# Optimization experiments

Measured on AMD Instinct MI355X. Metric: run time of the kernel, lower is better.

Reference implementation:

```python
import jax, jax.numpy as jnp
import numpy as np
from jax.scipy.linalg import solve_triangular

NUM_EMBEDDINGS = 512
EMBEDDING_DIM = 64
SPARSITY = 5
COMMITMENT = 0.25
EPS = 1e-10


def setup_inputs() -> dict:
    key = jax.random.key(0)
    k1, k2 = jax.random.split(key)
    z_e = jax.random.normal(k1, (64, EMBEDDING_DIM, 32, 32), dtype=jnp.float32)
    dictionary = jax.random.normal(k2, (EMBEDDING_DIM, NUM_EMBEDDINGS), dtype=jnp.float32)
    return {"z_e": z_e, "dictionary": dictionary}


def batch_omp(X, D, K):
    """Batched OMP with incremental Cholesky. X: (M, Bs), D: (M, N) col-normalized.
    Returns coefficients (N, Bs)."""
    N = D.shape[1]
    Bs = X.shape[1]
    G = D.T @ D                      # (N, N) Gram
    h_bar = (D.T @ X).T              # (Bs, N) correlations
    h = h_bar
    x = jnp.zeros_like(h_bar)        # dense coeff matrix, nonzero only on support
    I_logic = jnp.zeros((Bs, N), dtype=bool)
    L = jnp.ones((Bs, 1, 1), dtype=X.dtype)
    I = None
    b = jnp.arange(Bs)
    for k in range(1, K + 1):        # unrolled: K is a small static constant
        # pick most correlated unselected atom per sample
        index = jnp.argmax(jnp.abs(jnp.where(I_logic, 0.0, h)), axis=1)  # (Bs,)
        I_logic = I_logic.at[b, index].set(True)
        if k > 1:
            # incremental Cholesky update: L_new = [[L, 0], [w^T, sqrt(1 - |w|^2)]]
            G_stack = G[I, index[:, None]]                               # (Bs, k-1)
            w = solve_triangular(L, G_stack[..., None], lower=True)      # (Bs, k-1, 1)
            w_corner = jnp.sqrt(1.0 - jnp.sum(w ** 2, axis=1, keepdims=True))  # (Bs,1,1)
            top = jnp.concatenate([L, jnp.zeros((Bs, k - 1, 1), X.dtype)], axis=2)
            bot = jnp.concatenate([jnp.swapaxes(w, 1, 2), w_corner], axis=2)
            L = jnp.concatenate([top, bot], axis=1)                      # (Bs, k, k)
            I = jnp.concatenate([I, index[:, None]], axis=1)             # (Bs, k)
        else:
            I = index[:, None]
        # solve (L L^T) x_I = h_bar_I  (cholesky_solve)
        h_stack = jnp.take_along_axis(h_bar, I, axis=1)[..., None]       # (Bs, k, 1)
        y = solve_triangular(L, h_stack, lower=True)
        x_stack = solve_triangular(L, y, lower=True, trans=1)[..., 0]    # (Bs, k)
        # scatter support coefficients (indices are distinct per sample)
        x = jnp.zeros_like(h_bar).at[b[:, None], I].set(x_stack)
        beta = x @ G                                                     # (Bs, N)
        h = h_bar - beta
    return x.T                                                           # (N, Bs)


def reference(z_e, dictionary):
    B, C, H, W = z_e.shape
    signals = jnp.transpose(z_e, (0, 2, 3, 1)).reshape(-1, C).T          # (C, B*H*W)
    # F.normalize(dictionary, p=2, dim=0, eps)
    d_norm = dictionary / jnp.maximum(
        jnp.linalg.norm(dictionary, axis=0, keepdims=True), EPS)
    # sparse coding is done under no_grad in the original
    coeffs = jax.lax.stop_gradient(
        batch_omp(jax.lax.stop_gradient(signals),
                  jax.lax.stop_gradient(d_norm), SPARSITY))              # (N, B*H*W)
    recon = (d_norm @ coeffs).T                                          # (B*H*W, C)
    z_dl = jnp.transpose(recon.reshape(B, H, W, C), (0, 3, 1, 2))
    dl_latent_loss = jnp.mean((z_dl - jax.lax.stop_gradient(z_e)) ** 2)
    e_latent_loss = jnp.mean((jax.lax.stop_gradient(z_dl) - z_e) ** 2)
    loss = dl_latent_loss + COMMITMENT * e_latent_loss
    # straight-through estimator
    z_dl_st = z_e + jax.lax.stop_gradient(z_dl - z_e)
    return z_dl_st, loss, coeffs
```

## Files before the change

### kernel.cpp

```cpp
#include <hip/hip_runtime.h>
#include <type_traits>

#define N_ATOMS 512
#define C_DIM   64
#define K_SP    5
#define TS      16
#define HSTR    20


__global__ __launch_bounds__(256) void prep_norm_k(const float* __restrict__ dict,
                                                   float* __restrict__ dn,
                                                   float* __restrict__ dnT,
                                                   double* __restrict__ lossAcc) {
#pragma clang fp contract(off)
  const int n = blockIdx.x * 256 + threadIdx.x;
  if (blockIdx.x == 0 && threadIdx.x == 0) *lossAcc = 0.0;
  if (n >= N_ATOMS) return;
  float s = 0.0f;
  for (int c = 0; c < C_DIM; ++c) {
    float v = dict[c * N_ATOMS + n];
    float sq = v * v;
    s = s + sq;
  }
  float m = fmaxf(sqrtf(s), 1e-10f);
  for (int c = 0; c < C_DIM; ++c) {
    float q = dict[c * N_ATOMS + n] / m;
    dn[c * N_ATOMS + n] = q;
    dnT[n * C_DIM + c] = q;
  }
}

__global__ __launch_bounds__(256) void prep_gram_k(const float* __restrict__ dn,
                                                   float* __restrict__ G) {
#pragma clang fp contract(off)
  __shared__ float As[64][64];
  __shared__ float Bs[64][64];
  const int bi = blockIdx.x & 7, bj = blockIdx.x >> 3;
  const int tid = threadIdx.x;
  for (int r = 0; r < 16; ++r) {
    int e = r * 256 + tid;
    int c = e >> 6, i = e & 63;
    As[c][i] = dn[c * N_ATOMS + bi * 64 + i];
    Bs[c][i] = dn[c * N_ATOMS + bj * 64 + i];
  }
  __syncthreads();
  const int ti = tid & 15, tj = tid >> 4;
  float acc[4][4] = {};
  for (int c = 0; c < 64; ++c) {
    float a[4], b[4];
#pragma unroll
    for (int u = 0; u < 4; ++u) { a[u] = As[c][ti * 4 + u]; b[u] = Bs[c][tj * 4 + u]; }
#pragma unroll
    for (int u = 0; u < 4; ++u)
#pragma unroll
      for (int v = 0; v < 4; ++v) acc[u][v] = fmaf(a[u], b[v], acc[u][v]);
  }
  for (int u = 0; u < 4; ++u)
    for (int v = 0; v < 4; ++v)
      G[(size_t)(bi * 64 + ti * 4 + u) * N_ATOMS + bj * 64 + tj * 4 + v] = acc[u][v];
}

__global__ __launch_bounds__(256) void omp_main_k(const float* __restrict__ z,
                                                  const float* __restrict__ dn,
                                                  const float* __restrict__ dnT,
                                                  const float* __restrict__ Gm,
                                                  float* __restrict__ out0,
                                                  float* __restrict__ coeffs,
                                                  double* __restrict__ lossAcc) {
#pragma clang fp contract(off)
  __shared__ float Xs[64][16];
  __shared__ __align__(16) float UB[N_ATOMS * HSTR];
  __shared__ int   IldsI[TS][K_SP];
  __shared__ float IldsX[TS][K_SP];

  const int tid   = threadIdx.x;
  const int sbase = blockIdx.x * TS;
  const int b     = sbase >> 10;
  const int hw0   = sbase & 1023;
  const float* zb = z + (size_t)b * 65536;

  {
    int c = tid >> 2, slc = (tid & 3) * 4;
    float4 v = *reinterpret_cast<const float4*>(zb + c * 1024 + hw0 + slc);
    *reinterpret_cast<float4*>(&Xs[c][slc]) = v;
  }

  const int ia4 = (tid & 63) * 4;
  const int js4 = (tid >> 6) * 4;
  float acc[8][4] = {};
#pragma unroll
  for (int cc = 0; cc < 4; ++cc) {
    __syncthreads();
    {
      const float* src = dn + cc * 8192;
#pragma unroll
      for (int r = 0; r < 8; ++r) {
        int off = (r * 256 + tid) * 4;
        *reinterpret_cast<float4*>(&UB[off]) = *reinterpret_cast<const float4*>(src + off);
      }
    }
    __syncthreads();
#pragma unroll
    for (int c = 0; c < 16; ++c) {
      const float4 xv = *reinterpret_cast<const float4*>(&Xs[cc * 16 + c][js4]);
      const float4 d0 = *reinterpret_cast<const float4*>(&UB[c * 512 + ia4]);
      const float4 d1 = *reinterpret_cast<const float4*>(&UB[c * 512 + 256 + ia4]);
      const float dv[8] = { d0.x, d0.y, d0.z, d0.w, d1.x, d1.y, d1.z, d1.w };
      const float xw[4] = { xv.x, xv.y, xv.z, xv.w };
#pragma unroll
      for (int r = 0; r < 8; ++r)
#pragma unroll
        for (int u = 0; u < 4; ++u)
          acc[r][u] = fmaf(dv[r], xw[u], acc[r][u]);
    }
  }
  __syncthreads();
#pragma unroll
  for (int r = 0; r < 8; ++r) {
    int n = (r < 4) ? (ia4 + r) : (256 + ia4 + (r - 4));
    *reinterpret_cast<float4*>(&UB[n * HSTR + js4]) =
        make_float4(acc[r][0], acc[r][1], acc[r][2], acc[r][3]);
  }
  __syncthreads();

  const int lane = tid & 63;
  const int wid  = tid >> 6;
  double lsum = 0.0;

  for (int q = 0; q < 4; ++q) {
    const int sl = wid * 4 + q;
    float hb[8];
#pragma unroll
    for (int jb = 0; jb < 8; ++jb) hb[jb] = UB[(lane + 64 * jb) * HSTR + sl];

    unsigned selmask = 0;
    int   I[K_SP];
    float xs[K_SP];
    float hstk[K_SP];
    float Lm[K_SP][K_SP];
    int   srtI[4];
    float GrowS[4][8];

    auto iter = [&](auto KC) {
      constexpr int k = decltype(KC)::value;
      float cur[8];
      if constexpr (k == 1) {
#pragma unroll
        for (int jb = 0; jb < 8; ++jb) cur[jb] = hb[jb];
      } else {
        float xsS[k - 1];
#pragma unroll
        for (int u = 0; u < k - 1; ++u) {
          float xv = 0.0f;
#pragma unroll
          for (int t = 0; t < k - 1; ++t) xv = (I[t] == srtI[u]) ? xs[t] : xv;
          xsS[u] = xv;
        }
#pragma unroll
        for (int jb = 0; jb < 8; ++jb) {
          float beta = 0.0f;
#pragma unroll
          for (int u = 0; u < k - 1; ++u) beta = fmaf(xsS[u], GrowS[u][jb], beta);
          cur[jb] = hb[jb] - beta;
        }
      }
      float bv = -1.0f; int bn = 1 << 30;
#pragma unroll
      for (int jb = 0; jb < 8; ++jb) {
        float v = ((selmask >> jb) & 1u) ? 0.0f : fabsf(cur[jb]);
        int n = lane + 64 * jb;
        bool better = (v > bv) || ((v == bv) && (n < bn));
        bv = better ? v : bv; bn = better ? n : bn;
      }
#pragma unroll
      for (int m = 1; m < 64; m <<= 1) {
        float ov = __shfl_xor(bv, m, 64);
        int   on = __shfl_xor(bn, m, 64);
        bool better = (ov > bv) || ((ov == bv) && (on < bn));
        bv = better ? ov : bv; bn = better ? on : bn;
      }
      const int nsel = bn;
      I[k - 1] = nsel;
      if ((nsel & 63) == lane) selmask |= (1u << (nsel >> 6));

      if constexpr (k > 1) {
        float Gs[k - 1], w[k - 1];
#pragma unroll
        for (int t = 0; t < k - 1; ++t) Gs[t] = Gm[(size_t)I[t] * N_ATOMS + nsel];
#pragma unroll
        for (int t = 0; t < k - 1; ++t) {
          float a = Gs[t];
#pragma unroll
          for (int u = 0; u < t; ++u) a = a - Lm[t][u] * w[u];
          w[t] = a / Lm[t][t];
        }
        float ss = 0.0f;
#pragma unroll
        for (int t = 0; t < k - 1; ++t) { float sq = w[t] * w[t]; ss = ss + sq; }
        float wc = sqrtf(1.0f - ss);
#pragma unroll
        for (int t = 0; t < k - 1; ++t) Lm[k - 1][t] = w[t];
        Lm[k - 1][k - 1] = wc;
      } else {
        Lm[0][0] = 1.0f;
      }
      hstk[k - 1] = UB[nsel * HSTR + sl];
      float y[k];
#pragma unroll
      for (int t = 0; t < k; ++t) {
        float a = hstk[t];
#pragma unroll
        for (int u = 0; u < t; ++u) a = a - Lm[t][u] * y[u];
        y[t] = a / Lm[t][t];
      }
#pragma unroll
      for (int t = k - 1; t >= 0; --t) {
        float a = y[t];
#pragma unroll
        for (int u = t + 1; u < k; ++u) a = a - Lm[u][t] * xs[u];
        xs[t] = a / Lm[t][t];
      }
      if constexpr (k <= 4) {
        float nr[8];
#pragma unroll
        for (int jb = 0; jb < 8; ++jb) nr[jb] = Gm[(size_t)nsel * N_ATOMS + lane + 64 * jb];
        int p = 0;
#pragma unroll
        for (int u = 0; u < k - 1; ++u) p += (srtI[u] < nsel) ? 1 : 0;
#pragma unroll
        for (int u = k - 1; u >= 1; --u) {
          bool tp = (u > p);
          srtI[u] = tp ? srtI[u - 1] : srtI[u];
#pragma unroll
          for (int jb = 0; jb < 8; ++jb) GrowS[u][jb] = tp ? GrowS[u - 1][jb] : GrowS[u][jb];
        }
#pragma unroll
        for (int u = 0; u < k; ++u) {
          bool at = (u == p);
          srtI[u] = at ? nsel : srtI[u];
#pragma unroll
          for (int jb = 0; jb < 8; ++jb) GrowS[u][jb] = at ? nr[jb] : GrowS[u][jb];
        }
      }
    };
    iter(std::integral_constant<int, 1>{});
    iter(std::integral_constant<int, 2>{});
    iter(std::integral_constant<int, 3>{});
    iter(std::integral_constant<int, 4>{});
    iter(std::integral_constant<int, 5>{});

    if (lane == 0) {
#pragma unroll
      for (int t = 0; t < K_SP; ++t) { IldsI[sl][t] = I[t]; IldsX[sl][t] = xs[t]; }
    }

    int sI[5]; float sX[5];
#pragma unroll
    for (int t = 0; t < 5; ++t) { sI[t] = I[t]; sX[t] = xs[t]; }
#pragma unroll
    for (int a = 0; a < 4; ++a)
#pragma unroll
      for (int t = 0; t < 4 - a; ++t) {
        bool sw = sI[t] > sI[t + 1];
        int   i0 = sw ? sI[t + 1] : sI[t];
        int   i1 = sw ? sI[t] : sI[t + 1];
        float x0 = sw ? sX[t + 1] : sX[t];
        float x1 = sw ? sX[t] : sX[t + 1];
        sI[t] = i0; sI[t + 1] = i1; sX[t] = x0; sX[t + 1] = x1;
      }
    float r = 0.0f;
#pragma unroll
    for (int t = 0; t < 5; ++t) r = fmaf(sX[t], dnT[(size_t)sI[t] * C_DIM + lane], r);
    float ze = Xs[lane][sl];
    float t1 = r - ze;
    out0[(size_t)b * 65536 + lane * 1024 + hw0 + sl] = ze + t1;
    float sq = t1 * t1;
    lsum += (double)sq;
  }

#pragma unroll
  for (int m = 1; m < 64; m <<= 1) lsum += __shfl_xor(lsum, m, 64);
  if (lane == 0) atomicAdd(lossAcc, lsum);

  __syncthreads();
  {
    int rbase = tid >> 2;
    int c0 = (tid & 3) * 4;
#pragma unroll
    for (int p = 0; p < 8; ++p) {
      int rown = p * 64 + rbase;
      float v[4];
#pragma unroll
      for (int u = 0; u < 4; ++u) {
        int slc = c0 + u;
        float val = 0.0f;
#pragma unroll
        for (int t = 0; t < K_SP; ++t)
          val = (IldsI[slc][t] == rown) ? IldsX[slc][t] : val;
        v[u] = val;
      }
      size_t base = (size_t)rown * 65536 + sbase + c0;
      coeffs[base + 0] = v[0];
      coeffs[base + 1] = v[1];
      coeffs[base + 2] = v[2];
      coeffs[base + 3] = v[3];
    }
  }
}

__global__ void finalize_k(const double* __restrict__ lossAcc, float* __restrict__ out) {
  if (threadIdx.x == 0) {
    float dl = (float)(*lossAcc / 4194304.0);
    out[4194304] = dl + 0.25f * dl;
  }
}

extern "C" void kernel_launch(void* const* d_in, const int* in_sizes, int n_in,
                              void* d_out, int out_size, void* d_ws, size_t ws_size,
                              hipStream_t stream) {
  (void)in_sizes; (void)n_in; (void)out_size; (void)ws_size;
  const float* z    = (const float*)d_in[0];
  const float* dict = (const float*)d_in[1];
  float* out    = (float*)d_out;
  float* coeffs = out + 4194305;
  float* dn  = (float*)d_ws;
  float* dnT = dn + 32768;
  float* G   = dnT + 32768;
  double* lossAcc = (double*)((char*)d_ws + 1310720);

  prep_norm_k<<<2, 256, 0, stream>>>(dict, dn, dnT, lossAcc);
  prep_gram_k<<<64, 256, 0, stream>>>(dn, G);
  omp_main_k<<<4096, 256, 0, stream>>>(z, dn, dnT, G, out, coeffs, lossAcc);
  finalize_k<<<1, 64, 0, stream>>>(lossAcc, out);
}
```

Baseline: 485.8 us.

## Shrink LDS footprint, load dictionary via global_load_lds, fuse finalize via last-block counter

Changes the correlation buffer from atom-major with 20-float stride to sample-major rows of 520 floats, sized TS*520 instead of 512*20, and adds launch_bounds(256,4) so more blocks can be resident. Dictionary chunks now go straight from global memory to LDS with global_load_lds, and the forward triangular solve becomes incremental so only the newest y entry is computed each step. Coefficient stores become float4, the normalize kernel transposes through shared memory for coalesced dnT writes, and the finalize kernel is folded into the main kernel through an atomic block counter. These trade some atomic and fence overhead plus register pressure from the occupancy hint for fewer launches and cheaper memory traffic.

```diff
diff --git a/kernel.cpp b/kernel.cpp
--- a/kernel.cpp
+++ b/kernel.cpp
@@ -5,28 +5,39 @@
 #define C_DIM   64
 #define K_SP    5
 #define TS      16
-#define HSTR    20
-
-
-__global__ __launch_bounds__(256) void prep_norm_k(const float* __restrict__ dict,
-                                                   float* __restrict__ dn,
-                                                   float* __restrict__ dnT,
-                                                   double* __restrict__ lossAcc) {
+#define HROW    520
+
+
+__global__ __launch_bounds__(64) void prep_norm_k(const float* __restrict__ dict,
+                                                  float* __restrict__ dn,
+                                                  float* __restrict__ dnT,
+                                                  double* __restrict__ lossAcc,
+                                                  unsigned int* __restrict__ cnt) {
 #pragma clang fp contract(off)
-  const int n = blockIdx.x * 256 + threadIdx.x;
-  if (blockIdx.x == 0 && threadIdx.x == 0) *lossAcc = 0.0;
-  if (n >= N_ATOMS) return;
+  __shared__ float tile[64][65];
+  const int t = threadIdx.x;
+  const int n0 = blockIdx.x * 64;
+  const int n = n0 + t;
+  if (blockIdx.x == 0 && t == 0) { *lossAcc = 0.0; *cnt = 0u; }
   float s = 0.0f;
   for (int c = 0; c < C_DIM; ++c) {
     float v = dict[c * N_ATOMS + n];
+    tile[t][c] = v;
     float sq = v * v;
     s = s + sq;
   }
   float m = fmaxf(sqrtf(s), 1e-10f);
   for (int c = 0; c < C_DIM; ++c) {
-    float q = dict[c * N_ATOMS + n] / m;
+    float q = tile[t][c] / m;
+    tile[t][c] = q;
     dn[c * N_ATOMS + n] = q;
-    dnT[n * C_DIM + c] = q;
+  }
+  __syncthreads();
+  for (int r = 0; r < 16; ++r) {
+    int e = r * 64 + t;
+    int nn = e >> 4, cc = (e & 15) * 4;
+    float4 v = make_float4(tile[nn][cc], tile[nn][cc + 1], tile[nn][cc + 2], tile[nn][cc + 3]);
+    *reinterpret_cast<float4*>(&dnT[(size_t)(n0 + nn) * C_DIM + cc]) = v;
   }
 }
 
@@ -60,16 +71,17 @@
       G[(size_t)(bi * 64 + ti * 4 + u) * N_ATOMS + bj * 64 + tj * 4 + v] = acc[u][v];
 }
 
-__global__ __launch_bounds__(256) void omp_main_k(const float* __restrict__ z,
-                                                  const float* __restrict__ dn,
-                                                  const float* __restrict__ dnT,
-                                                  const float* __restrict__ Gm,
-                                                  float* __restrict__ out0,
-                                                  float* __restrict__ coeffs,
-                                                  double* __restrict__ lossAcc) {
+__global__ __launch_bounds__(256, 4) void omp_main_k(const float* __restrict__ z,
+                                                     const float* __restrict__ dn,
+                                                     const float* __restrict__ dnT,
+                                                     const float* __restrict__ Gm,
+                                                     float* __restrict__ out0,
+                                                     float* __restrict__ coeffs,
+                                                     double* __restrict__ lossAcc,
+                                                     unsigned int* __restrict__ cnt) {
 #pragma clang fp contract(off)
   __shared__ float Xs[64][16];
-  __shared__ __align__(16) float UB[N_ATOMS * HSTR];
+  __shared__ __align__(16) float UB[TS * HROW];
   __shared__ int   IldsI[TS][K_SP];
   __shared__ float IldsX[TS][K_SP];
 
@@ -96,7 +108,10 @@
 #pragma unroll
       for (int r = 0; r < 8; ++r) {
         int off = (r * 256 + tid) * 4;
-        *reinterpret_cast<float4*>(&UB[off]) = *reinterpret_cast<const float4*>(src + off);
+        __builtin_amdgcn_global_load_lds(
+            (const __attribute__((address_space(1))) unsigned int*)(src + off),
+            (__attribute__((address_space(3))) unsigned int*)(&UB[off]),
+            16, 0, 0);
       }
     }
     __syncthreads();
@@ -116,10 +131,12 @@
   }
   __syncthreads();
 #pragma unroll
-  for (int r = 0; r < 8; ++r) {
-    int n = (r < 4) ? (ia4 + r) : (256 + ia4 + (r - 4));
-    *reinterpret_cast<float4*>(&UB[n * HSTR + js4]) =
-        make_float4(acc[r][0], acc[r][1], acc[r][2], acc[r][3]);
+  for (int u = 0; u < 4; ++u) {
+    const int sl = js4 + u;
+    *reinterpret_cast<float4*>(&UB[sl * HROW + ia4]) =
+        make_float4(acc[0][u], acc[1][u], acc[2][u], acc[3][u]);
+    *reinterpret_cast<float4*>(&UB[sl * HROW + 256 + ia4]) =
+        make_float4(acc[4][u], acc[5][u], acc[6][u], acc[7][u]);
   }
   __syncthreads();
 
@@ -131,12 +148,13 @@
     const int sl = wid * 4 + q;
     float hb[8];
 #pragma unroll
-    for (int jb = 0; jb < 8; ++jb) hb[jb] = UB[(lane + 64 * jb) * HSTR + sl];
+    for (int jb = 0; jb < 8; ++jb) hb[jb] = UB[sl * HROW + lane + 64 * jb];
 
     unsigned selmask = 0;
     int   I[K_SP];
     float xs[K_SP];
     float hstk[K_SP];
+    float yv[K_SP];
     float Lm[K_SP][K_SP];
     int   srtI[4];
     float GrowS[4][8];
@@ -204,18 +222,16 @@
       } else {
         Lm[0][0] = 1.0f;
       }
-      hstk[k - 1] = UB[nsel * HSTR + sl];
-      float y[k];
-#pragma unroll
-      for (int t = 0; t < k; ++t) {
-        float a = hstk[t];
-#pragma unroll
-        for (int u = 0; u < t; ++u) a = a - Lm[t][u] * y[u];
-        y[t] = a / Lm[t][t];
+      hstk[k - 1] = UB[sl * HROW + nsel];
+      {
+        float a = hstk[k - 1];
+#pragma unroll
+        for (int u = 0; u < k - 1; ++u) a = a - Lm[k - 1][u] * yv[u];
+        yv[k - 1] = a / Lm[k - 1][k - 1];
       }
 #pragma unroll
       for (int t = k - 1; t >= 0; --t) {
-        float a = y[t];
+        float a = yv[t];
 #pragma unroll
         for (int u = t + 1; u < k; ++u) a = a - Lm[u][t] * xs[u];
         xs[t] = a / Lm[t][t];
@@ -299,19 +315,20 @@
           val = (IldsI[slc][t] == rown) ? IldsX[slc][t] : val;
         v[u] = val;
       }
-      size_t base = (size_t)rown * 65536 + sbase + c0;
-      coeffs[base + 0] = v[0];
-      coeffs[base + 1] = v[1];
-      coeffs[base + 2] = v[2];
-      coeffs[base + 3] = v[3];
-    }
-  }
-}
-
-__global__ void finalize_k(const double* __restrict__ lossAcc, float* __restrict__ out) {
-  if (threadIdx.x == 0) {
-    float dl = (float)(*lossAcc / 4194304.0);
-    out[4194304] = dl + 0.25f * dl;
+      *reinterpret_cast<float4*>(&coeffs[(size_t)rown * 65536 + sbase + c0]) =
+          make_float4(v[0], v[1], v[2], v[3]);
+    }
+  }
+
+  if (tid == 0) {
+    __threadfence();
+    unsigned int old = atomicAdd(cnt, 1u);
+    if (old == (unsigned int)(gridDim.x - 1)) {
+      __threadfence();
+      double tot = atomicAdd(lossAcc, 0.0);
+      float dl = (float)(tot / 4194304.0);
+      out0[4194304] = dl + 0.25f * dl;
+    }
   }
 }
 
@@ -327,9 +344,9 @@
   float* dnT = dn + 32768;
   float* G   = dnT + 32768;
   double* lossAcc = (double*)((char*)d_ws + 1310720);
-
-  prep_norm_k<<<2, 256, 0, stream>>>(dict, dn, dnT, lossAcc);
+  unsigned int* cnt = (unsigned int*)((char*)d_ws + 1310728);
+
+  prep_norm_k<<<8, 64, 0, stream>>>(dict, dn, dnT, lossAcc, cnt);
   prep_gram_k<<<64, 256, 0, stream>>>(dn, G);
-  omp_main_k<<<4096, 256, 0, stream>>>(z, dn, dnT, G, out, coeffs, lossAcc);
-  finalize_k<<<1, 64, 0, stream>>>(lossAcc, out);
+  omp_main_k<<<4096, 256, 0, stream>>>(z, dn, dnT, G, out, coeffs, lossAcc, cnt);
 }
```

After: 644.3 us. +32.6%, slower.
